# Kernel tuning notes

Measured on AMD Instinct MI355X. Metric: run time of the kernel, lower is better.

The kernel has to match this reference:

```python
import math
import jax, jax.numpy as jnp
import numpy as np

TOPK = 2
CAPACITY_FACTOR = 1.25
MIN_CAPACITY = 4


def setup_inputs() -> dict:
    key = jax.random.key(0)
    k1, k2, k3, k4, k5 = jax.random.split(key, 5)
    B, T, H, W, D = 2, 8, 16, 16, 2048
    E, I = 16, 2048
    s = 1.0 / math.sqrt(D)
    return {
        "hidden_states": jax.random.normal(k1, (B, T, H, W, D), dtype=jnp.float32),
        "wg_weight": jax.random.normal(k2, (E, D), dtype=jnp.float32) * s,
        "gate_proj": jax.random.normal(k3, (E, I, D), dtype=jnp.float32) * s,
        "up_proj": jax.random.normal(k4, (E, I, D), dtype=jnp.float32) * s,
        "down_proj": jax.random.normal(k5, (E, D, I), dtype=jnp.float32) * (1.0 / math.sqrt(I)),
    }


def _moe_forward(x, wg, gp, up, dp):
    B, T, H, W, D = x.shape
    S = T * H * W
    # core_shape=(1,1,1): indexing tokens == calculate tokens, flatten (T,H,W)
    tokens = x.reshape(B, S, D).transpose(1, 0, 2).reshape(-1, D)  # (N, D)
    N = tokens.shape[0]
    E = wg.shape[0]

    logits = tokens.astype(jnp.float32) @ wg.T              # (N, E)
    gates = jax.nn.softmax(logits, axis=1)                  # (N, E)

    # static expert capacity: topk * max(ceil(N/E * cf), min_capacity)
    cap = TOPK * max(math.ceil(N / E * CAPACITY_FACTOR), MIN_CAPACITY)

    _, expert_index = jax.lax.top_k(gates, TOPK)            # (N, k)
    expert_mask = jax.nn.one_hot(expert_index, E, dtype=jnp.int32)  # (N, k, E)

    # aux load-balance loss (computed for fidelity)
    mask_aux = expert_mask.max(axis=1).astype(jnp.float32)  # (N, E)
    l_aux = (E ** 2) * jnp.mean(jnp.mean(mask_aux, axis=0) * jnp.mean(gates, axis=0))

    # normalize top-k probabilities (norm_topk_prob=True, topk>1)
    gates_s = jnp.clip(jnp.einsum('nke,ne->n', expert_mask.astype(gates.dtype), gates),
                       jnp.finfo(gates.dtype).eps)
    router_probs = gates / gates_s[:, None]                 # (N, E)

    # token priority: cumsum over (topk*N) flattened in topk-major order
    em = expert_mask.transpose(1, 0, 2).reshape(TOPK * N, E)  # (kN, E)
    tp = jnp.cumsum(em, axis=0) * em - 1
    tp = tp.reshape(TOPK, N, E).transpose(1, 0, 2).max(axis=1)  # (N, E)
    valid = (tp >= 0) & (tp < cap)
    tp = jnp.where(valid, tp, 0)
    dispatch_mask = (tp[:, :, None] == jnp.arange(cap)[None, None, :]) & valid[:, :, None]  # (N,E,C) bool
    combine_weights = router_probs[:, :, None] * dispatch_mask  # (N, E, C)

    # dispatch -> expert FFN (SwiGLU) -> combine
    dm = dispatch_mask.astype(tokens.dtype)
    dispatched = jnp.einsum('nec,nd->ecd', dm, tokens)      # (E, C, D)
    gate_out = jax.nn.silu(jnp.einsum('ecd,eid->eci', dispatched, gp))
    up_out = jnp.einsum('ecd,eid->eci', dispatched, up)
    expert_out = jnp.einsum('eci,edi->ecd', gate_out * up_out, dp)  # (E, C, D)
    combined = jnp.einsum('nec,ecd->nd', combine_weights, expert_out)  # (N, D)

    y = combined.reshape(S, B, D).transpose(1, 0, 2).reshape(B, T, H, W, D)
    return y, l_aux


def reference(hidden_states, wg_weight, gate_proj, up_proj, down_proj):
    y, _l_aux = _moe_forward(hidden_states, wg_weight, gate_proj, up_proj, down_proj)
    return y
```

## Files before the change

### kernel.cpp

```cpp
#include <hip/hip_runtime.h>
#include <hip/hip_bf16.h>
#include <cstdint>
#include <cstddef>

#define NTOK 4096
#define NEXP 16
#define DIM  2048
#define IDIM 2048
#define CAP  640
#define SEQ  2048

typedef float v4f __attribute__((ext_vector_type(4)));
typedef short v8s __attribute__((ext_vector_type(8)));

__device__ __forceinline__ unsigned short f2b(float x) {
    union { float f; unsigned u; } c; c.f = x;
    unsigned r = c.u + 0x7FFFu + ((c.u >> 16) & 1u);
    return (unsigned short)(r >> 16);
}
__device__ __forceinline__ float b2f(unsigned short x) {
    union { unsigned u; float f; } c; c.u = ((unsigned)x) << 16;
    return c.f;
}

__device__ __forceinline__ void async16(const void* g, void* l) {
    __builtin_amdgcn_global_load_lds(
        (const __attribute__((address_space(1))) unsigned int*)g,
        (__attribute__((address_space(3))) unsigned int*)l,
        16, 0, 0);
}

__global__ __launch_bounds__(256) void router_kernel(
    const float* __restrict__ hidden, const float* __restrict__ wg,
    int* __restrict__ top1, int* __restrict__ top2,
    float* __restrict__ w1, float* __restrict__ w2)
{
    int wid  = threadIdx.x >> 6;
    int lane = threadIdx.x & 63;
    int n = blockIdx.x * 4 + wid;
    int e = lane & 15;
    int chunk = lane >> 4;
    const float* tok  = hidden + ((size_t)(n & 1) * SEQ + (n >> 1)) * DIM;
    const float* wrow = wg + (size_t)e * DIM;
    float acc = 0.f;
    int d0 = chunk * (DIM / 4);
    #pragma unroll 4
    for (int d = d0; d < d0 + DIM / 4; d += 4) {
        float4 t4 = *(const float4*)(tok + d);
        float4 g4 = *(const float4*)(wrow + d);
        acc += t4.x * g4.x + t4.y * g4.y + t4.z * g4.z + t4.w * g4.w;
    }
    acc += __shfl_down(acc, 32);
    acc += __shfl_down(acc, 16);
    float v = acc;
    float v1 = v; int i1 = e;
    #pragma unroll
    for (int off = 8; off; off >>= 1) {
        float ov = __shfl_xor(v1, off);
        int   oi = __shfl_xor(i1, off);
        if (ov > v1 || (ov == v1 && oi < i1)) { v1 = ov; i1 = oi; }
    }
    float v2 = (e == i1) ? -INFINITY : v; int i2 = e;
    #pragma unroll
    for (int off = 8; off; off >>= 1) {
        float ov = __shfl_xor(v2, off);
        int   oi = __shfl_xor(i2, off);
        if (ov > v2 || (ov == v2 && oi < i2)) { v2 = ov; i2 = oi; }
    }
    if (lane == 0) {
        float e2v = expf(v2 - v1);
        float inv = 1.f / (1.f + e2v);
        top1[n] = i1; top2[n] = i2;
        w1[n] = inv;  w2[n] = e2v * inv;
    }
}

__global__ __launch_bounds__(1024) void slot_kernel(
    const int* __restrict__ top1, const int* __restrict__ top2,
    int* __restrict__ slot1, int* __restrict__ slot2,
    int* __restrict__ exp_tok, int* __restrict__ counts)
{
    int w = threadIdx.x >> 6;
    int lane = threadIdx.x & 63;
    unsigned long long below = (lane == 0) ? 0ull : ((~0ull) >> (64 - lane));
    int base = 0;
    for (int c = 0; c < NTOK / 64; ++c) {
        int n = c * 64 + lane;
        bool p = (top1[n] == w);
        unsigned long long m = __ballot(p);
        if (p) {
            int s = base + __popcll(m & below);
            slot1[n] = s;
            if (s < CAP) exp_tok[w * CAP + s] = n;
        }
        base += __popcll(m);
    }
    for (int c = 0; c < NTOK / 64; ++c) {
        int n = c * 64 + lane;
        bool p = (top2[n] == w);
        unsigned long long m = __ballot(p);
        if (p) {
            int s = base + __popcll(m & below);
            slot2[n] = s;
            if (s < CAP) exp_tok[w * CAP + s] = n;
        }
        base += __popcll(m);
    }
    if (lane == 0) counts[w] = base < CAP ? base : CAP;
}

__global__ __launch_bounds__(256) void dispatch_kernel(
    const float* __restrict__ hidden, const int* __restrict__ exp_tok,
    const int* __restrict__ counts, unsigned short* __restrict__ disp)
{
    int s = blockIdx.x, e = blockIdx.y;
    unsigned short* dst = disp + ((size_t)e * CAP + s) * DIM + threadIdx.x * 8;
    if (s < counts[e]) {
        int n = exp_tok[e * CAP + s];
        const float* src = hidden + ((size_t)(n & 1) * SEQ + (n >> 1)) * DIM + threadIdx.x * 8;
        float4 a = *(const float4*)src;
        float4 b = *(const float4*)(src + 4);
        v8s o;
        o[0] = (short)f2b(a.x); o[1] = (short)f2b(a.y);
        o[2] = (short)f2b(a.z); o[3] = (short)f2b(a.w);
        o[4] = (short)f2b(b.x); o[5] = (short)f2b(b.y);
        o[6] = (short)f2b(b.z); o[7] = (short)f2b(b.w);
        *(v8s*)dst = o;
    } else {
        v8s z = {0, 0, 0, 0, 0, 0, 0, 0};
        *(v8s*)dst = z;
    }
}

#define BM 128
#define BN 128
#define BK 64

__device__ __forceinline__ void stage_tile(
    const unsigned short* __restrict__ gbase, int grow0, int k0, int rs,
    unsigned short* lds, int wv, int ln)
{
    int sr = ln >> 3;
    int cb = ln & 7;
    #pragma unroll
    for (int p = 0; p < 4; ++p) {
        int r = p * 32 + wv * 8 + sr;
        const unsigned short* g = gbase + (size_t)(grow0 + r) * rs + k0 + ((cb ^ (r & 7)) << 3);
        async16(g, lds + (p * 32 + wv * 8) * 64);
    }
}

__device__ __forceinline__ void issue_b(
    const float* __restrict__ gbase, int grow0, int k0, int rs,
    float4 (&regs)[8], int tid)
{
    int cb = tid & 7;
    int r0 = tid >> 3;
    #pragma unroll
    for (int p = 0; p < 4; ++p) {
        const float* g = gbase + (size_t)(grow0 + p * 32 + r0) * rs + k0 + (cb << 3);
        regs[2 * p]     = *(const float4*)g;
        regs[2 * p + 1] = *(const float4*)(g + 4);
    }
}

__device__ __forceinline__ void write_b(
    const float4 (&regs)[8], unsigned short* lds, int tid)
{
    int cb = tid & 7;
    int r0 = tid >> 3;
    #pragma unroll
    for (int p = 0; p < 4; ++p) {
        int r = p * 32 + r0;
        float4 x = regs[2 * p], y = regs[2 * p + 1];
        v8s o;
        o[0] = (short)f2b(x.x); o[1] = (short)f2b(x.y);
        o[2] = (short)f2b(x.z); o[3] = (short)f2b(x.w);
        o[4] = (short)f2b(y.x); o[5] = (short)f2b(y.y);
        o[6] = (short)f2b(y.z); o[7] = (short)f2b(y.w);
        *(v8s*)&lds[r * 64 + ((cb ^ (r & 7)) << 3)] = o;
    }
}

__device__ __forceinline__ void grid_decomp(int bid, int& mi, int& ni, int& e) {
    int swz = (bid & 7) * 160 + (bid >> 3);
    mi = swz % 5;
    int t = swz / 5;
    ni = t & 15;
    e  = t >> 4;
}

__global__ __launch_bounds__(256, 2) void gateup_kernel(
    const unsigned short* __restrict__ disp, const float* __restrict__ gp,
    const float* __restrict__ up, const int* __restrict__ counts,
    unsigned short* __restrict__ hbuf)
{
    __shared__ unsigned short As[2][BM * BK];
    __shared__ unsigned short Bgs[BN * BK];
    __shared__ unsigned short Bus[BN * BK];
    int mi, ni, e;
    grid_decomp(blockIdx.x, mi, ni, e);
    int m0 = mi * BM;
    if (m0 >= counts[e]) return;
    int n0 = ni * BN;
    int tid = threadIdx.x;
    int wv = tid >> 6, ln = tid & 63;
    int wm = wv & 1, wn = wv >> 1;
    int lrow = ln & 15, quad = ln >> 4;
    int sw = lrow & 7;

    const unsigned short* Ab = disp + (size_t)e * CAP * DIM;
    const float* Gb = gp + (size_t)e * IDIM * DIM;
    const float* Ub = up + (size_t)e * IDIM * DIM;

    int arow[4], brow[4];
    #pragma unroll
    for (int i = 0; i < 4; ++i) {
        arow[i] = (wm * 64 + i * 16 + lrow) * 64;
        brow[i] = (wn * 64 + i * 16 + lrow) * 64;
    }

    v4f accg[4][4], accu[4][4];
    #pragma unroll
    for (int i = 0; i < 4; ++i)
        #pragma unroll
        for (int j = 0; j < 4; ++j) { accg[i][j] = (v4f)0.f; accu[i][j] = (v4f)0.f; }

    float4 rg[8], ru[8];
    stage_tile(Ab, m0, 0, DIM, As[0], wv, ln);
    issue_b(Gb, n0, 0, DIM, rg, tid);
    issue_b(Ub, n0, 0, DIM, ru, tid);

    for (int k0 = 0; k0 < DIM; k0 += BK) {
        int cur = (k0 >> 6) & 1;
        __syncthreads();
        write_b(rg, Bgs, tid);
        write_b(ru, Bus, tid);
        __syncthreads();
        int kn = k0 + BK;
        if (kn < DIM) {
            stage_tile(Ab, m0, kn, DIM, As[cur ^ 1], wv, ln);
            issue_b(Gb, n0, kn, DIM, rg, tid);
            issue_b(Ub, n0, kn, DIM, ru, tid);
        }
        #pragma unroll
        for (int ks = 0; ks < BK; ks += 32) {
            int cq = ks >> 3;
            v8s a[4];
            #pragma unroll
            for (int i = 0; i < 4; ++i)
                a[i] = *(const v8s*)&As[cur][arow[i] + (((cq + quad) ^ sw) << 3)];
            #pragma unroll
            for (int j = 0; j < 4; ++j) {
                v8s bg = *(const v8s*)&Bgs[brow[j] + (((cq + quad) ^ sw) << 3)];
                v8s bu = *(const v8s*)&Bus[brow[j] + (((cq + quad) ^ sw) << 3)];
                #pragma unroll
                for (int i = 0; i < 4; ++i) {
                    accg[i][j] = __builtin_amdgcn_mfma_f32_16x16x32_bf16(a[i], bg, accg[i][j], 0, 0, 0);
                    accu[i][j] = __builtin_amdgcn_mfma_f32_16x16x32_bf16(a[i], bu, accu[i][j], 0, 0, 0);
                }
            }
        }
    }
    unsigned short* hb = hbuf + (size_t)e * CAP * IDIM;
    #pragma unroll
    for (int i = 0; i < 4; ++i)
        #pragma unroll
        for (int j = 0; j < 4; ++j) {
            int row = m0 + wm * 64 + i * 16 + quad * 4;
            int col = n0 + wn * 64 + j * 16 + lrow;
            #pragma unroll
            for (int rg_ = 0; rg_ < 4; ++rg_) {
                float g = accg[i][j][rg_], u = accu[i][j][rg_];
                float hv = (g / (1.f + __expf(-g))) * u;
                hb[(size_t)(row + rg_) * IDIM + col] = f2b(hv);
            }
        }
}

__global__ __launch_bounds__(256, 2) void down_kernel(
    const unsigned short* __restrict__ hbuf, const float* __restrict__ dp,
    const int* __restrict__ counts, unsigned short* __restrict__ eo)
{
    __shared__ unsigned short As[2][BM * BK];
    __shared__ unsigned short Bs[BN * BK];
    int mi, ni, e;
    grid_decomp(blockIdx.x, mi, ni, e);
    int m0 = mi * BM;
    if (m0 >= counts[e]) return;
    int n0 = ni * BN;
    int tid = threadIdx.x;
    int wv = tid >> 6, ln = tid & 63;
    int wm = wv & 1, wn = wv >> 1;
    int lrow = ln & 15, quad = ln >> 4;
    int sw = lrow & 7;

    const unsigned short* Ab = hbuf + (size_t)e * CAP * IDIM;
    const float* Db = dp + (size_t)e * DIM * IDIM;

    int arow[4], brow[4];
    #pragma unroll
    for (int i = 0; i < 4; ++i) {
        arow[i] = (wm * 64 + i * 16 + lrow) * 64;
        brow[i] = (wn * 64 + i * 16 + lrow) * 64;
    }

    v4f acc[4][4];
    #pragma unroll
    for (int i = 0; i < 4; ++i)
        #pragma unroll
        for (int j = 0; j < 4; ++j) acc[i][j] = (v4f)0.f;

    float4 rb[8];
    stage_tile(Ab, m0, 0, IDIM, As[0], wv, ln);
    issue_b(Db, n0, 0, IDIM, rb, tid);

    for (int k0 = 0; k0 < IDIM; k0 += BK) {
        int cur = (k0 >> 6) & 1;
        __syncthreads();
        write_b(rb, Bs, tid);
        __syncthreads();
        int kn = k0 + BK;
        if (kn < IDIM) {
            stage_tile(Ab, m0, kn, IDIM, As[cur ^ 1], wv, ln);
            issue_b(Db, n0, kn, IDIM, rb, tid);
        }
        #pragma unroll
        for (int ks = 0; ks < BK; ks += 32) {
            int cq = ks >> 3;
            v8s a[4];
            #pragma unroll
            for (int i = 0; i < 4; ++i)
                a[i] = *(const v8s*)&As[cur][arow[i] + (((cq + quad) ^ sw) << 3)];
            #pragma unroll
            for (int j = 0; j < 4; ++j) {
                v8s b = *(const v8s*)&Bs[brow[j] + (((cq + quad) ^ sw) << 3)];
                #pragma unroll
                for (int i = 0; i < 4; ++i)
                    acc[i][j] = __builtin_amdgcn_mfma_f32_16x16x32_bf16(a[i], b, acc[i][j], 0, 0, 0);
            }
        }
    }
    unsigned short* ob = eo + (size_t)e * CAP * DIM;
    #pragma unroll
    for (int i = 0; i < 4; ++i)
        #pragma unroll
        for (int j = 0; j < 4; ++j) {
            int row = m0 + wm * 64 + i * 16 + quad * 4;
            int col = n0 + wn * 64 + j * 16 + lrow;
            #pragma unroll
            for (int rg_ = 0; rg_ < 4; ++rg_)
                ob[(size_t)(row + rg_) * DIM + col] = f2b(acc[i][j][rg_]);
        }
}

__global__ __launch_bounds__(256) void combine_kernel(
    const unsigned short* __restrict__ eo,
    const int* __restrict__ top1, const int* __restrict__ top2,
    const int* __restrict__ slot1, const int* __restrict__ slot2,
    const float* __restrict__ w1, const float* __restrict__ w2,
    float* __restrict__ out)
{
    int n = blockIdx.x;
    int d = threadIdx.x * 8;
    float acc[8];
    #pragma unroll
    for (int i = 0; i < 8; ++i) acc[i] = 0.f;
    int s1 = slot1[n], s2 = slot2[n];
    if (s1 < CAP) {
        const unsigned short* p = eo + ((size_t)top1[n] * CAP + s1) * DIM + d;
        float w = w1[n];
        v8s v = *(const v8s*)p;
        #pragma unroll
        for (int i = 0; i < 8; ++i) acc[i] += w * b2f((unsigned short)v[i]);
    }
    if (s2 < CAP) {
        const unsigned short* p = eo + ((size_t)top2[n] * CAP + s2) * DIM + d;
        float w = w2[n];
        v8s v = *(const v8s*)p;
        #pragma unroll
        for (int i = 0; i < 8; ++i) acc[i] += w * b2f((unsigned short)v[i]);
    }
    float* o = out + ((size_t)(n & 1) * SEQ + (n >> 1)) * DIM + d;
    float4 o0 = {acc[0], acc[1], acc[2], acc[3]};
    float4 o1 = {acc[4], acc[5], acc[6], acc[7]};
    *(float4*)o = o0;
    *(float4*)(o + 4) = o1;
}

extern "C" void kernel_launch(void* const* d_in, const int* in_sizes, int n_in,
                              void* d_out, int out_size, void* d_ws, size_t ws_size,
                              hipStream_t stream) {
    const float* hidden = (const float*)d_in[0];
    const float* wg     = (const float*)d_in[1];
    const float* gp     = (const float*)d_in[2];
    const float* up     = (const float*)d_in[3];
    const float* dp     = (const float*)d_in[4];
    float* out = (float*)d_out;
    char* ws = (char*)d_ws;

    int*   top1    = (int*)(ws + 0);
    int*   top2    = (int*)(ws + 16384);
    float* w1      = (float*)(ws + 32768);
    float* w2      = (float*)(ws + 49152);
    int*   slot1   = (int*)(ws + 65536);
    int*   slot2   = (int*)(ws + 81920);
    int*   counts  = (int*)(ws + 98304);
    int*   exp_tok = (int*)(ws + 98560);
    unsigned short* disp = (unsigned short*)(ws + 262144);
    unsigned short* hbuf = (unsigned short*)(ws + 262144 + 41943040ull);
    unsigned short* eo   = (unsigned short*)(ws + 262144 + 2ull*41943040ull);

    const int NB = (CAP / BM) * (IDIM / BN) * NEXP;

    router_kernel<<<NTOK / 4, 256, 0, stream>>>(hidden, wg, top1, top2, w1, w2);
    slot_kernel<<<1, 1024, 0, stream>>>(top1, top2, slot1, slot2, exp_tok, counts);
    dispatch_kernel<<<dim3(CAP, NEXP), 256, 0, stream>>>(hidden, exp_tok, counts, disp);
    gateup_kernel<<<NB, 256, 0, stream>>>(disp, gp, up, counts, hbuf);
    down_kernel<<<NB, 256, 0, stream>>>(hbuf, dp, counts, eo);
    combine_kernel<<<NTOK, 256, 0, stream>>>(eo, top1, top2, slot1, slot2, w1, w2, out);
}
```

Baseline: 1.097 ms.

## Enlarge expert GEMM M-tile to 256 rows to cut fp32 weight re-reads

Raises the token-row tile of the gate/up and down expert GEMMs from 128 to 256, which cuts the capacity dimension from 5 to 3 tiles. Gate/up now runs 512-thread blocks with 8 waves. Down keeps 256 threads but gives each wave 8x4 accumulators. The aim is fewer re-reads and bf16 conversions of the large fp32 weight matrices per expert. The cost is dynamic shared memory of 96KB/80KB, which likely limits blocks per CU. The last tile now overhangs CAP, so stores are bounds-guarded and loads read past the expert slice. Fewer blocks and higher register pressure may reduce latency hiding.

```diff
diff --git a/kernel.cpp b/kernel.cpp
--- a/kernel.cpp
+++ b/kernel.cpp
@@ -132,46 +132,47 @@
     }
 }
 
-#define BM 128
-#define BN 128
 #define BK 64
 
-__device__ __forceinline__ void stage_tile(
+template<int NW, int ROUNDS>
+__device__ __forceinline__ void stage_a(
     const unsigned short* __restrict__ gbase, int grow0, int k0, int rs,
     unsigned short* lds, int wv, int ln)
 {
     int sr = ln >> 3;
     int cb = ln & 7;
     #pragma unroll
-    for (int p = 0; p < 4; ++p) {
-        int r = p * 32 + wv * 8 + sr;
+    for (int p = 0; p < ROUNDS; ++p) {
+        int r = p * (NW * 8) + wv * 8 + sr;
         const unsigned short* g = gbase + (size_t)(grow0 + r) * rs + k0 + ((cb ^ (r & 7)) << 3);
-        async16(g, lds + (p * 32 + wv * 8) * 64);
-    }
-}
-
-__device__ __forceinline__ void issue_b(
+        async16(g, lds + (p * (NW * 8) + wv * 8) * 64);
+    }
+}
+
+template<int NT, int ROUNDS>
+__device__ __forceinline__ void issue_bx(
     const float* __restrict__ gbase, int grow0, int k0, int rs,
-    float4 (&regs)[8], int tid)
+    float4* regs, int tid)
 {
     int cb = tid & 7;
     int r0 = tid >> 3;
     #pragma unroll
-    for (int p = 0; p < 4; ++p) {
-        const float* g = gbase + (size_t)(grow0 + p * 32 + r0) * rs + k0 + (cb << 3);
+    for (int p = 0; p < ROUNDS; ++p) {
+        const float* g = gbase + (size_t)(grow0 + p * (NT / 8) + r0) * rs + k0 + (cb << 3);
         regs[2 * p]     = *(const float4*)g;
         regs[2 * p + 1] = *(const float4*)(g + 4);
     }
 }
 
-__device__ __forceinline__ void write_b(
-    const float4 (&regs)[8], unsigned short* lds, int tid)
+template<int NT, int ROUNDS>
+__device__ __forceinline__ void write_bx(
+    const float4* regs, unsigned short* lds, int tid)
 {
     int cb = tid & 7;
     int r0 = tid >> 3;
     #pragma unroll
-    for (int p = 0; p < 4; ++p) {
-        int r = p * 32 + r0;
+    for (int p = 0; p < ROUNDS; ++p) {
+        int r = p * (NT / 8) + r0;
         float4 x = regs[2 * p], y = regs[2 * p + 1];
         v8s o;
         o[0] = (short)f2b(x.x); o[1] = (short)f2b(x.y);
@@ -182,30 +183,32 @@
     }
 }
 
-__device__ __forceinline__ void grid_decomp(int bid, int& mi, int& ni, int& e) {
-    int swz = (bid & 7) * 160 + (bid >> 3);
-    mi = swz % 5;
-    int t = swz / 5;
+__device__ __forceinline__ void grid_decomp3(int bid, int& mi, int& ni, int& e) {
+    int swz = (bid & 7) * 96 + (bid >> 3);
+    mi = swz % 3;
+    int t = swz / 3;
     ni = t & 15;
     e  = t >> 4;
 }
 
-__global__ __launch_bounds__(256, 2) void gateup_kernel(
+__global__ __launch_bounds__(512, 2) void gateup_kernel(
     const unsigned short* __restrict__ disp, const float* __restrict__ gp,
     const float* __restrict__ up, const int* __restrict__ counts,
     unsigned short* __restrict__ hbuf)
 {
-    __shared__ unsigned short As[2][BM * BK];
-    __shared__ unsigned short Bgs[BN * BK];
-    __shared__ unsigned short Bus[BN * BK];
+    extern __shared__ unsigned short smem[];
+    unsigned short* As0 = smem;
+    unsigned short* As1 = smem + 16384;
+    unsigned short* Bgs = smem + 32768;
+    unsigned short* Bus = smem + 40960;
     int mi, ni, e;
-    grid_decomp(blockIdx.x, mi, ni, e);
-    int m0 = mi * BM;
+    grid_decomp3(blockIdx.x, mi, ni, e);
+    int m0 = mi * 256;
     if (m0 >= counts[e]) return;
-    int n0 = ni * BN;
+    int n0 = ni * 128;
     int tid = threadIdx.x;
     int wv = tid >> 6, ln = tid & 63;
-    int wm = wv & 1, wn = wv >> 1;
+    int wm = wv >> 1, wn = wv & 1;
     int lrow = ln & 15, quad = ln >> 4;
     int sw = lrow & 7;
 
@@ -226,22 +229,24 @@
         #pragma unroll
         for (int j = 0; j < 4; ++j) { accg[i][j] = (v4f)0.f; accu[i][j] = (v4f)0.f; }
 
-    float4 rg[8], ru[8];
-    stage_tile(Ab, m0, 0, DIM, As[0], wv, ln);
-    issue_b(Gb, n0, 0, DIM, rg, tid);
-    issue_b(Ub, n0, 0, DIM, ru, tid);
+    float4 rg[4], ru[4];
+    stage_a<8, 4>(Ab, m0, 0, DIM, As0, wv, ln);
+    issue_bx<512, 2>(Gb, n0, 0, DIM, rg, tid);
+    issue_bx<512, 2>(Ub, n0, 0, DIM, ru, tid);
 
     for (int k0 = 0; k0 < DIM; k0 += BK) {
         int cur = (k0 >> 6) & 1;
+        unsigned short* Ac = cur ? As1 : As0;
+        unsigned short* An = cur ? As0 : As1;
         __syncthreads();
-        write_b(rg, Bgs, tid);
-        write_b(ru, Bus, tid);
+        write_bx<512, 2>(rg, Bgs, tid);
+        write_bx<512, 2>(ru, Bus, tid);
         __syncthreads();
         int kn = k0 + BK;
         if (kn < DIM) {
-            stage_tile(Ab, m0, kn, DIM, As[cur ^ 1], wv, ln);
-            issue_b(Gb, n0, kn, DIM, rg, tid);
-            issue_b(Ub, n0, kn, DIM, ru, tid);
+            stage_a<8, 4>(Ab, m0, kn, DIM, An, wv, ln);
+            issue_bx<512, 2>(Gb, n0, kn, DIM, rg, tid);
+            issue_bx<512, 2>(Ub, n0, kn, DIM, ru, tid);
         }
         #pragma unroll
         for (int ks = 0; ks < BK; ks += 32) {
@@ -249,7 +254,7 @@
             v8s a[4];
             #pragma unroll
             for (int i = 0; i < 4; ++i)
-                a[i] = *(const v8s*)&As[cur][arow[i] + (((cq + quad) ^ sw) << 3)];
+                a[i] = *(const v8s*)&Ac[arow[i] + (((cq + quad) ^ sw) << 3)];
             #pragma unroll
             for (int j = 0; j < 4; ++j) {
                 v8s bg = *(const v8s*)&Bgs[brow[j] + (((cq + quad) ^ sw) << 3)];
@@ -271,9 +276,11 @@
             int col = n0 + wn * 64 + j * 16 + lrow;
             #pragma unroll
             for (int rg_ = 0; rg_ < 4; ++rg_) {
-                float g = accg[i][j][rg_], u = accu[i][j][rg_];
-                float hv = (g / (1.f + __expf(-g))) * u;
-                hb[(size_t)(row + rg_) * IDIM + col] = f2b(hv);
+                if (row + rg_ < CAP) {
+                    float g = accg[i][j][rg_], u = accu[i][j][rg_];
+                    float hv = (g / (1.f + __expf(-g))) * u;
+                    hb[(size_t)(row + rg_) * IDIM + col] = f2b(hv);
+                }
             }
         }
 }
@@ -282,75 +289,82 @@
     const unsigned short* __restrict__ hbuf, const float* __restrict__ dp,
     const int* __restrict__ counts, unsigned short* __restrict__ eo)
 {
-    __shared__ unsigned short As[2][BM * BK];
-    __shared__ unsigned short Bs[BN * BK];
+    extern __shared__ unsigned short smem[];
+    unsigned short* As0 = smem;
+    unsigned short* As1 = smem + 16384;
+    unsigned short* Bs  = smem + 32768;
     int mi, ni, e;
-    grid_decomp(blockIdx.x, mi, ni, e);
-    int m0 = mi * BM;
+    grid_decomp3(blockIdx.x, mi, ni, e);
+    int m0 = mi * 256;
     if (m0 >= counts[e]) return;
-    int n0 = ni * BN;
+    int n0 = ni * 128;
     int tid = threadIdx.x;
     int wv = tid >> 6, ln = tid & 63;
-    int wm = wv & 1, wn = wv >> 1;
+    int wm = wv >> 1, wn = wv & 1;
     int lrow = ln & 15, quad = ln >> 4;
     int sw = lrow & 7;
 
     const unsigned short* Ab = hbuf + (size_t)e * CAP * IDIM;
     const float* Db = dp + (size_t)e * DIM * IDIM;
 
-    int arow[4], brow[4];
-    #pragma unroll
-    for (int i = 0; i < 4; ++i) {
-        arow[i] = (wm * 64 + i * 16 + lrow) * 64;
-        brow[i] = (wn * 64 + i * 16 + lrow) * 64;
-    }
-
-    v4f acc[4][4];
-    #pragma unroll
-    for (int i = 0; i < 4; ++i)
+    int arow[8], brow[4];
+    #pragma unroll
+    for (int i = 0; i < 8; ++i)
+        arow[i] = (wm * 128 + i * 16 + lrow) * 64;
+    #pragma unroll
+    for (int j = 0; j < 4; ++j)
+        brow[j] = (wn * 64 + j * 16 + lrow) * 64;
+
+    v4f acc[8][4];
+    #pragma unroll
+    for (int i = 0; i < 8; ++i)
         #pragma unroll
         for (int j = 0; j < 4; ++j) acc[i][j] = (v4f)0.f;
 
     float4 rb[8];
-    stage_tile(Ab, m0, 0, IDIM, As[0], wv, ln);
-    issue_b(Db, n0, 0, IDIM, rb, tid);
+    stage_a<4, 8>(Ab, m0, 0, IDIM, As0, wv, ln);
+    issue_bx<256, 4>(Db, n0, 0, IDIM, rb, tid);
 
     for (int k0 = 0; k0 < IDIM; k0 += BK) {
         int cur = (k0 >> 6) & 1;
+        unsigned short* Ac = cur ? As1 : As0;
+        unsigned short* An = cur ? As0 : As1;
         __syncthreads();
-        write_b(rb, Bs, tid);
+        write_bx<256, 4>(rb, Bs, tid);
         __syncthreads();
         int kn = k0 + BK;
         if (kn < IDIM) {
-            stage_tile(Ab, m0, kn, IDIM, As[cur ^ 1], wv, ln);
-            issue_b(Db, n0, kn, IDIM, rb, tid);
+            stage_a<4, 8>(Ab, m0, kn, IDIM, An, wv, ln);
+            issue_bx<256, 4>(Db, n0, kn, IDIM, rb, tid);
         }
         #pragma unroll
         for (int ks = 0; ks < BK; ks += 32) {
             int cq = ks >> 3;
-            v8s a[4];
-            #pragma unroll
-            for (int i = 0; i < 4; ++i)
-                a[i] = *(const v8s*)&As[cur][arow[i] + (((cq + quad) ^ sw) << 3)];
+            v8s a[8];
+            #pragma unroll
+            for (int i = 0; i < 8; ++i)
+                a[i] = *(const v8s*)&Ac[arow[i] + (((cq + quad) ^ sw) << 3)];
             #pragma unroll
             for (int j = 0; j < 4; ++j) {
                 v8s b = *(const v8s*)&Bs[brow[j] + (((cq + quad) ^ sw) << 3)];
                 #pragma unroll
-                for (int i = 0; i < 4; ++i)
+                for (int i = 0; i < 8; ++i)
                     acc[i][j] = __builtin_amdgcn_mfma_f32_16x16x32_bf16(a[i], b, acc[i][j], 0, 0, 0);
             }
         }
     }
     unsigned short* ob = eo + (size_t)e * CAP * DIM;
     #pragma unroll
-    for (int i = 0; i < 4; ++i)
+    for (int i = 0; i < 8; ++i)
         #pragma unroll
         for (int j = 0; j < 4; ++j) {
-            int row = m0 + wm * 64 + i * 16 + quad * 4;
+            int row = m0 + wm * 128 + i * 16 + quad * 4;
             int col = n0 + wn * 64 + j * 16 + lrow;
             #pragma unroll
-            for (int rg_ = 0; rg_ < 4; ++rg_)
-                ob[(size_t)(row + rg_) * DIM + col] = f2b(acc[i][j][rg_]);
+            for (int rg_ = 0; rg_ < 4; ++rg_) {
+                if (row + rg_ < CAP)
+                    ob[(size_t)(row + rg_) * DIM + col] = f2b(acc[i][j][rg_]);
+            }
         }
 }
 
@@ -411,12 +425,21 @@
     unsigned short* hbuf = (unsigned short*)(ws + 262144 + 41943040ull);
     unsigned short* eo   = (unsigned short*)(ws + 262144 + 2ull*41943040ull);
 
-    const int NB = (CAP / BM) * (IDIM / BN) * NEXP;
+    static bool attr_set = false;
+    if (!attr_set) {
+        hipFuncSetAttribute((const void*)gateup_kernel,
+                            hipFuncAttributeMaxDynamicSharedMemorySize, 98304);
+        hipFuncSetAttribute((const void*)down_kernel,
+                            hipFuncAttributeMaxDynamicSharedMemorySize, 81920);
+        attr_set = true;
+    }
+
+    const int NB = 3 * 16 * NEXP;
 
     router_kernel<<<NTOK / 4, 256, 0, stream>>>(hidden, wg, top1, top2, w1, w2);
     slot_kernel<<<1, 1024, 0, stream>>>(top1, top2, slot1, slot2, exp_tok, counts);
     dispatch_kernel<<<dim3(CAP, NEXP), 256, 0, stream>>>(hidden, exp_tok, counts, disp);
-    gateup_kernel<<<NB, 256, 0, stream>>>(disp, gp, up, counts, hbuf);
-    down_kernel<<<NB, 256, 0, stream>>>(hbuf, dp, counts, eo);
+    gateup_kernel<<<NB, 512, 98304, stream>>>(disp, gp, up, counts, hbuf);
+    down_kernel<<<NB, 256, 81920, stream>>>(hbuf, dp, counts, eo);
     combine_kernel<<<NTOK, 256, 0, stream>>>(eo, top1, top2, slot1, slot2, w1, w2, out);
 }
```

Measured after the change: 1.048 ms. 4.5% less time.
